# Kernel optimization log

Measured on AMD Instinct MI355X. Metric: run time of the kernel, lower is better.

The kernel has to match this reference:

```python
import jax, jax.numpy as jnp
import numpy as np

B, S, D = 8, 1024, 1024

def setup_inputs() -> dict:
    key = jax.random.key(0)
    ks = jax.random.split(key, 6)
    context = jax.random.normal(ks[0], (B, S, D), dtype=jnp.float32)
    eos_mask = jax.random.randint(ks[1], (B, S), 0, 2, dtype=jnp.int32)
    prior = jax.random.uniform(ks[2], (), dtype=jnp.float32)
    adj_mat = jax.random.randint(ks[3], (B, S, S), 0, 2, dtype=jnp.int32)
    Wk = jax.random.normal(ks[4], (D, D), dtype=jnp.float32) * 0.02
    Wq = jax.random.normal(ks[5], (D, D), dtype=jnp.float32) * 0.02
    bk = jnp.zeros((D,), jnp.float32)
    bq = jnp.zeros((D,), jnp.float32)
    ln_gamma = jnp.ones((D,), jnp.float32)
    ln_beta = jnp.zeros((D,), jnp.float32)
    return {"context": context, "eos_mask": eos_mask, "prior": prior,
            "adj_mat": adj_mat, "Wk": Wk, "bk": bk, "Wq": Wq, "bq": bq,
            "ln_gamma": ln_gamma, "ln_beta": ln_beta}

def reference(context, eos_mask, prior, adj_mat, Wk, bk, Wq, bq, ln_gamma, ln_beta):
    d_model = context.shape[-1]
    seq_len = context.shape[1]
    # LayerNorm (annotated-transformer style: unbiased std, eps added to std)
    mu = jnp.mean(context, axis=-1, keepdims=True)
    std = jnp.std(context, axis=-1, keepdims=True, ddof=1)
    x = ln_gamma * (context - mu) / (std + 1e-6) + ln_beta
    # projections (torch Linear: x @ W.T + b)
    key_p = x @ Wk.T + bk
    query = x @ Wq.T + bq
    scores = jnp.einsum('bqd,bkd->bqk', query, key_p) / (d_model / 2)
    scores = jnp.where(adj_mat == 0, -1e9, scores)
    neibor_attn = jax.nn.softmax(scores, axis=-1)
    neibor_attn = jnp.sqrt(neibor_attn * jnp.swapaxes(neibor_attn, -1, -2) + 1e-9)
    neibor_attn = prior + (1.0 - prior) * neibor_attn
    # constant structural matrices
    a = jnp.eye(seq_len, k=1, dtype=jnp.float32)          # superdiagonal
    b = jnp.eye(seq_len, dtype=jnp.float32)               # diagonal
    tri = jnp.triu(jnp.ones((seq_len, seq_len), jnp.float32))  # upper incl diag
    # t = (log(attn+eps) masked to superdiagonal) @ tri
    t = jnp.matmul(jnp.where(a == 0, 0.0, jnp.log(neibor_attn + 1e-9)), tri)
    g_attn = jnp.exp(jnp.matmul(tri, t))
    g_attn = jnp.where((tri - b) == 0, 0.0, g_attn)  # keep strict upper only
    g_attn = g_attn + jnp.swapaxes(g_attn, -1, -2) + jnp.where(b == 0, 1e-9, neibor_attn)
    return (g_attn, neibor_attn)
```

## Files before the change

### kernel.cpp

```cpp
#include <hip/hip_runtime.h>
#include <hip/hip_bf16.h>

#define S_LEN 1024
#define D_DIM 1024
#define N_BAT 8
#define BSS   (8ull*1024ull*1024ull)

using bf16x8 = __attribute__((ext_vector_type(8))) short;
using f32x4  = __attribute__((ext_vector_type(4))) float;

__device__ __forceinline__ short f2bf(float v) {
    __hip_bfloat16 h = __float2bfloat16(v);
    return *reinterpret_cast<short*>(&h);
}

__device__ __forceinline__ void gload_lds16(const void* g, void* l) {
    __builtin_amdgcn_global_load_lds(
        (const __attribute__((address_space(1))) void*)g,
        (__attribute__((address_space(3))) void*)l, 16, 0, 0);
}

template<int KITERS>
__device__ __forceinline__ void gemm_mainloop256(
    const short* __restrict__ A, const short* __restrict__ Bt,
    int brow, int bcol, int kstart,
    short* As, short* Bs, f32x4 acc[4][4])
{
    const int tid  = threadIdx.x;
    const int lane = tid & 63;
    const int w    = tid >> 6;
    const int wr   = w >> 1;
    const int wc   = w & 1;
    const int rsel = lane & 15;
    const int kb   = (lane >> 4) * 16;
    const int sw   = (rsel & 7) << 4;

    const int srow  = tid >> 3;
    const int scolb = ((tid & 7) * 16) ^ ((srow & 7) << 4);
    const int sdst  = tid * 16;

#pragma unroll
    for (int m = 0; m < 4; ++m)
#pragma unroll
        for (int n = 0; n < 4; ++n) acc[m][n] = 0.0f;

    auto stage = [&](int slot, int k0) {
        char* Ad = (char*)As + slot * 32768;
        char* Bd = (char*)Bs + slot * 16384;
#pragma unroll
        for (int c = 0; c < 4; ++c) {
            const int row = c * 64 + srow;
            gload_lds16((const char*)(A + (size_t)(brow + row) * 1024 + k0) + scolb,
                        Ad + c * 8192 + sdst);
        }
#pragma unroll
        for (int c = 0; c < 2; ++c) {
            const int row = c * 64 + srow;
            gload_lds16((const char*)(Bt + (size_t)(bcol + row) * 1024 + k0) + scolb,
                        Bd + c * 8192 + sdst);
        }
    };

    stage(0, kstart);
    if (KITERS > 1) stage(1, kstart + 64);

#pragma unroll
    for (int t = 0; t < KITERS; ++t) {
        if (t < KITERS - 1) asm volatile("s_waitcnt vmcnt(6)" ::: "memory");
        else                asm volatile("s_waitcnt vmcnt(0)" ::: "memory");
        __builtin_amdgcn_s_barrier();
        asm volatile("" ::: "memory");

        const char* Ac = (const char*)As + (t % 3) * 32768;
        const char* Bc = (const char*)Bs + (t % 3) * 16384;
        bf16x8 af[4][2], bfr[4][2];
#pragma unroll
        for (int m = 0; m < 4; ++m) {
            const int row = wr * 64 + m * 16 + rsel;
#pragma unroll
            for (int kk = 0; kk < 2; ++kk)
                af[m][kk] = *(const bf16x8*)&Ac[row * 128 + ((kk * 64 + kb) ^ sw)];
        }
#pragma unroll
        for (int n = 0; n < 4; ++n) {
            const int row = wc * 64 + n * 16 + rsel;
#pragma unroll
            for (int kk = 0; kk < 2; ++kk)
                bfr[n][kk] = *(const bf16x8*)&Bc[row * 128 + ((kk * 64 + kb) ^ sw)];
        }

        if (t + 2 < KITERS) stage((t + 2) % 3, kstart + (t + 2) * 64);

        __builtin_amdgcn_s_setprio(1);
#pragma unroll
        for (int kk = 0; kk < 2; ++kk)
#pragma unroll
            for (int m = 0; m < 4; ++m)
#pragma unroll
                for (int n = 0; n < 4; ++n)
                    acc[m][n] = __builtin_amdgcn_mfma_f32_16x16x32_bf16(
                        af[m][kk], bfr[n][kk], acc[m][n], 0, 0, 0);
        __builtin_amdgcn_s_setprio(0);
    }
}

__global__ __launch_bounds__(512) void gemm_bf16(
    const short* __restrict__ A, const short* __restrict__ Bt,
    short* __restrict__ C)
{
    __shared__ short As[3 * 16384];
    __shared__ short Bs[3 * 8192];
    const int flat = blockIdx.x + 32 * blockIdx.y;
    const int nid  = (flat & 7) * 32 + (flat >> 3);
    const int mx   = nid >> 3;
    const int ny   = nid & 7;
    const int brow = mx * 256, bcol = ny * 128;

    f32x4 acc[4][4];
    gemm_mainloop256<16>(A, Bt, brow, bcol, 0, As, Bs, acc);

    const int lane = threadIdx.x & 63;
    const int w    = threadIdx.x >> 6;
    const int wr   = w >> 1, wc = w & 1;
#pragma unroll
    for (int m = 0; m < 4; ++m)
#pragma unroll
        for (int n = 0; n < 4; ++n) {
            const int colg = bcol + wc * 64 + n * 16 + (lane & 15);
#pragma unroll
            for (int r = 0; r < 4; ++r) {
                const int rowg = brow + wr * 64 + m * 16 + ((lane >> 4) * 4 + r);
                C[(size_t)rowg * 1024 + colg] = f2bf(acc[m][n][r]);
            }
        }
}

__global__ __launch_bounds__(512) void gemm_scores(
    const short* __restrict__ Tm, const short* __restrict__ Xm,
    const float* __restrict__ p, const float* __restrict__ r2,
    const float* __restrict__ c0p, float* __restrict__ Sc)
{
    __shared__ short As[3 * 16384];
    __shared__ short Bs[3 * 8192];
    const int flat = blockIdx.x + 4 * blockIdx.y + 32 * blockIdx.z;
    const int nid  = (flat & 7) * 32 + (flat >> 3);
    const int b    = nid >> 5;
    const int rem  = nid & 31;
    const int mx   = rem & 3;
    const int ny   = rem >> 2;
    const short* A  = Tm + (size_t)b * 1024 * 1024;
    const short* Bt = Xm + (size_t)b * 1024 * 1024;
    const float* pb = p  + (size_t)b * 1024;
    const float* rb = r2 + (size_t)b * 1024;
    float* C = Sc + (size_t)b * 1024 * 1024;
    const int brow = mx * 256, bcol = ny * 128;

    f32x4 acc[4][4];
    gemm_mainloop256<16>(A, Bt, brow, bcol, 0, As, Bs, acc);

    const int lane = threadIdx.x & 63;
    const int w    = threadIdx.x >> 6;
    const int wr   = w >> 1, wc = w & 1;
    const float c0v = c0p[0];
#pragma unroll
    for (int m = 0; m < 4; ++m)
#pragma unroll
        for (int n = 0; n < 4; ++n) {
            const int colg = bcol + wc * 64 + n * 16 + (lane & 15);
            const float radd = rb[colg] + c0v;
#pragma unroll
            for (int r = 0; r < 4; ++r) {
                const int rowg = brow + wr * 64 + m * 16 + ((lane >> 4) * 4 + r);
                C[(size_t)rowg * 1024 + colg] =
                    (acc[m][n][r] + pb[rowg] + radd) * 0.001953125f;
            }
        }
}

__global__ __launch_bounds__(512) void gemm_splitk(
    const short* __restrict__ A, const short* __restrict__ Bt,
    float* __restrict__ P)
{
    __shared__ short As[3 * 16384];
    __shared__ short Bs[3 * 8192];
    const int brow = blockIdx.x * 256, bcol = blockIdx.y * 128;
    const int z = blockIdx.z;

    f32x4 acc[4][4];
    gemm_mainloop256<4>(A, Bt, brow, bcol, z * 256, As, Bs, acc);

    float* Pz = P + (size_t)z * 1024 * 1024;
    const int lane = threadIdx.x & 63;
    const int w    = threadIdx.x >> 6;
    const int wr   = w >> 1, wc = w & 1;
#pragma unroll
    for (int m = 0; m < 4; ++m)
#pragma unroll
        for (int n = 0; n < 4; ++n) {
            const int colg = bcol + wc * 64 + n * 16 + (lane & 15);
#pragma unroll
            for (int r = 0; r < 4; ++r) {
                const int rowg = brow + wr * 64 + m * 16 + ((lane >> 4) * 4 + r);
                Pz[(size_t)rowg * 1024 + colg] = acc[m][n][r];
            }
        }
}

__global__ __launch_bounds__(256) void reduce_m2t(
    const float* __restrict__ P, short* __restrict__ M)
{
    const int idx = blockIdx.x * 256 + threadIdx.x;
    const float4* P4 = (const float4*)P;
    float4 s = P4[idx];
    const float4 s1 = P4[idx + 262144];
    const float4 s2 = P4[idx + 524288];
    const float4 s3 = P4[idx + 786432];
    s.x += s1.x + s2.x + s3.x;
    s.y += s1.y + s2.y + s3.y;
    s.z += s1.z + s2.z + s3.z;
    s.w += s1.w + s2.w + s3.w;
    short4 o;
    o.x = f2bf(s.x); o.y = f2bf(s.y); o.z = f2bf(s.z); o.w = f2bf(s.w);
    ((short4*)M)[idx] = o;
}

__global__ __launch_bounds__(256) void bias_gemv1(
    const float* __restrict__ Wq, const float* __restrict__ Wk,
    const float* __restrict__ bk, const float* __restrict__ bq,
    float* __restrict__ pu, float* __restrict__ pv)
{
    __shared__ float su[8][128];
    __shared__ float sv[8][128];
    const int tx = threadIdx.x & 31;
    const int ty = threadIdx.x >> 5;
    const int colBase = blockIdx.x * 128;
    const int rowBase = blockIdx.y * 64;
    const int i = colBase + tx * 4;
    float4 au = {0,0,0,0}, av = {0,0,0,0};
#pragma unroll
    for (int jj = 0; jj < 8; ++jj) {
        const int j = rowBase + ty + jj * 8;
        const float bkv = bk[j], bqv = bq[j];
        const float4 wq = *(const float4*)&Wq[(size_t)j * 1024 + i];
        const float4 wk = *(const float4*)&Wk[(size_t)j * 1024 + i];
        au.x += wq.x * bkv; au.y += wq.y * bkv; au.z += wq.z * bkv; au.w += wq.w * bkv;
        av.x += wk.x * bqv; av.y += wk.y * bqv; av.z += wk.z * bqv; av.w += wk.w * bqv;
    }
    ((float4*)su[ty])[tx] = au;
    ((float4*)sv[ty])[tx] = av;
    __syncthreads();
    if (ty == 0) {
        float4 s1 = ((float4*)su[0])[tx];
        float4 s2 = ((float4*)sv[0])[tx];
#pragma unroll
        for (int k = 1; k < 8; ++k) {
            const float4 t1 = ((float4*)su[k])[tx];
            const float4 t2 = ((float4*)sv[k])[tx];
            s1.x += t1.x; s1.y += t1.y; s1.z += t1.z; s1.w += t1.w;
            s2.x += t2.x; s2.y += t2.y; s2.z += t2.z; s2.w += t2.w;
        }
        ((float4*)&pu[(size_t)blockIdx.y * 1024 + colBase])[tx] = s1;
        ((float4*)&pv[(size_t)blockIdx.y * 1024 + colBase])[tx] = s2;
    }
}

__global__ __launch_bounds__(256) void bias_gemv2(
    const float* __restrict__ pu, const float* __restrict__ pv,
    const float* __restrict__ bk, const float* __restrict__ bq,
    float* __restrict__ u, float* __restrict__ v, float* __restrict__ c0)
{
    __shared__ float sh[4];
    const int i = blockIdx.x * 256 + threadIdx.x;
    float su = 0.0f, sv = 0.0f;
#pragma unroll
    for (int k = 0; k < 16; ++k) {
        su += pu[k * 1024 + i];
        sv += pv[k * 1024 + i];
    }
    u[i] = su;
    v[i] = sv;
    if (blockIdx.x == 0) {
        const int t = threadIdx.x;
        const float4 a = ((const float4*)bq)[t];
        const float4 b = ((const float4*)bk)[t];
        float s = a.x*b.x + a.y*b.y + a.z*b.z + a.w*b.w;
        for (int off = 32; off > 0; off >>= 1) s += __shfl_down(s, off);
        const int lane = t & 63, w = t >> 6;
        if (lane == 0) sh[w] = s;
        __syncthreads();
        if (t == 0) c0[0] = sh[0] + sh[1] + sh[2] + sh[3];
    }
}

__global__ __launch_bounds__(256) void ln_kernel(
    const float* __restrict__ X, const float* __restrict__ gamma,
    const float* __restrict__ beta, const float* __restrict__ u,
    const float* __restrict__ v2, short* __restrict__ Y,
    float* __restrict__ p, float* __restrict__ r2)
{
    __shared__ float sh[16];
    const size_t row = blockIdx.x;
    const int t = threadIdx.x;
    float4 v = ((const float4*)(X + row * 1024))[t];
    float s  = v.x + v.y + v.z + v.w;
    float ss = v.x*v.x + v.y*v.y + v.z*v.z + v.w*v.w;
    for (int off = 32; off > 0; off >>= 1) {
        s  += __shfl_down(s, off);
        ss += __shfl_down(ss, off);
    }
    const int lane = t & 63, w = t >> 6;
    if (lane == 0) { sh[w] = s; sh[4 + w] = ss; }
    __syncthreads();
    if (t == 0) {
        float S  = sh[0] + sh[1] + sh[2] + sh[3];
        float SS = sh[4] + sh[5] + sh[6] + sh[7];
        float mu = S * (1.0f / 1024.0f);
        float var = fmaxf((SS - S * mu) * (1.0f / 1023.0f), 0.0f);
        sh[0] = mu;
        sh[1] = 1.0f / (sqrtf(var) + 1e-6f);
    }
    __syncthreads();
    const float mu = sh[0], inv = sh[1];
    float4 g  = ((const float4*)gamma)[t];
    float4 be = ((const float4*)beta)[t];
    float y0 = g.x * (v.x - mu) * inv + be.x;
    float y1 = g.y * (v.y - mu) * inv + be.y;
    float y2 = g.z * (v.z - mu) * inv + be.z;
    float y3 = g.w * (v.w - mu) * inv + be.w;
    short4 o;
    o.x = f2bf(y0); o.y = f2bf(y1); o.z = f2bf(y2); o.w = f2bf(y3);
    ((short4*)(Y + row * 1024))[t] = o;
    float4 uu = ((const float4*)u)[t];
    float4 vv = ((const float4*)v2)[t];
    float dp = y0*uu.x + y1*uu.y + y2*uu.z + y3*uu.w;
    float dr = y0*vv.x + y1*vv.y + y2*vv.z + y3*vv.w;
    for (int off = 32; off > 0; off >>= 1) {
        dp += __shfl_down(dp, off);
        dr += __shfl_down(dr, off);
    }
    if (lane == 0) { sh[8 + w] = dp; sh[12 + w] = dr; }
    __syncthreads();
    if (t == 0) {
        p[row]  = sh[8] + sh[9] + sh[10] + sh[11];
        r2[row] = sh[12] + sh[13] + sh[14] + sh[15];
    }
}

__global__ __launch_bounds__(256) void cvt_t_kernel(
    const float* __restrict__ Wq, const float* __restrict__ Wk,
    short* __restrict__ wqt, short* __restrict__ wkt)
{
    __shared__ float T[32][33];
    const float* src = blockIdx.z ? Wk : Wq;
    short* dst = blockIdx.z ? wkt : wqt;
    const int bi = blockIdx.x * 32, bj = blockIdx.y * 32;
    const int c = threadIdx.x & 31, r0 = threadIdx.x >> 5;
#pragma unroll
    for (int rr = 0; rr < 4; ++rr) {
        const int r = r0 + rr * 8;
        T[r][c] = src[(size_t)(bi + r) * 1024 + bj + c];
    }
    __syncthreads();
#pragma unroll
    for (int rr = 0; rr < 4; ++rr) {
        const int r = r0 + rr * 8;
        dst[(size_t)(bj + r) * 1024 + bi + c] = f2bf(T[c][r]);
    }
}

__global__ __launch_bounds__(256) void softmax_kernel(
    const float* __restrict__ Sc, const int* __restrict__ adj,
    float* __restrict__ At)
{
    __shared__ float sh[4];
    const size_t row = blockIdx.x;
    const int t = threadIdx.x;
    const float4 sv = ((const float4*)(Sc + row * 1024))[t];
    const int4   av = ((const int4*)(adj + row * 1024))[t];
    float m = -3.0e38f;
    if (av.x) m = fmaxf(m, sv.x);
    if (av.y) m = fmaxf(m, sv.y);
    if (av.z) m = fmaxf(m, sv.z);
    if (av.w) m = fmaxf(m, sv.w);
    for (int off = 32; off > 0; off >>= 1) m = fmaxf(m, __shfl_down(m, off));
    const int lane = t & 63, w = t >> 6;
    if (lane == 0) sh[w] = m;
    __syncthreads();
    const float M = fmaxf(fmaxf(sh[0], sh[1]), fmaxf(sh[2], sh[3]));
    __syncthreads();
    float e0 = av.x ? expf(sv.x - M) : 0.0f;
    float e1 = av.y ? expf(sv.y - M) : 0.0f;
    float e2 = av.z ? expf(sv.z - M) : 0.0f;
    float e3 = av.w ? expf(sv.w - M) : 0.0f;
    float s = e0 + e1 + e2 + e3;
    for (int off = 32; off > 0; off >>= 1) s += __shfl_down(s, off);
    if (lane == 0) sh[w] = s;
    __syncthreads();
    const float Sm = sh[0] + sh[1] + sh[2] + sh[3];
    float4 o;
    if (Sm > 0.0f) {
        const float inv = 1.0f / Sm;
        o.x = e0 * inv; o.y = e1 * inv; o.z = e2 * inv; o.w = e3 * inv;
    } else {
        o.x = o.y = o.z = o.w = 1.0f / 1024.0f;
    }
    ((float4*)(At + row * 1024))[t] = o;
}

__global__ __launch_bounds__(1024) void cum2_kernel(
    const float* __restrict__ At, const float* __restrict__ prior_p,
    double* __restrict__ cum)
{
    __shared__ double sh[1024];
    const int b = blockIdx.x;
    const int t = threadIdx.x;
    const float prior = *prior_p;
    const float om = 1.0f - prior;
    const float* attn = At + (size_t)b * 1024 * 1024;
    double v = 0.0;
    if (t >= 1) {
        const int k = t - 1;
        const float a1 = attn[(size_t)k * 1024 + (k + 1)];
        const float a2 = attn[(size_t)(k + 1) * 1024 + k];
        const float na = prior + om * sqrtf(a1 * a2 + 1e-9f);
        v = (double)logf(na + 1e-9f);
    }
    sh[t] = v;
    __syncthreads();
#pragma unroll
    for (int off = 1; off < 1024; off <<= 1) {
        const double add = (t >= off) ? sh[t - off] : 0.0;
        __syncthreads();
        sh[t] += add;
        __syncthreads();
    }
    cum[b * 1024 + t] = sh[t];
}

__global__ __launch_bounds__(256) void na_g_kernel(
    float* __restrict__ At, const float* __restrict__ prior_p,
    const double* __restrict__ cum, float* __restrict__ G)
{
    const int ti = blockIdx.x >> 5, tj = blockIdx.x & 31;
    if (tj < ti) return;
    const int b = blockIdx.y;
    const float prior = *prior_p;
    const float om = 1.0f - prior;
    float* base = At + (size_t)b * 1024 * 1024;
    float* gb   = G  + (size_t)b * 1024 * 1024;
    const double* cb = cum + (size_t)b * 1024;
    __shared__ float T1[32][33];
    __shared__ float T2[32][33];
    const int c = threadIdx.x & 31, r0 = threadIdx.x >> 5;
#pragma unroll
    for (int rr = 0; rr < 4; ++rr) {
        const int r = r0 + rr * 8;
        T1[r][c] = base[(size_t)(ti * 32 + r) * 1024 + tj * 32 + c];
        T2[r][c] = base[(size_t)(tj * 32 + r) * 1024 + ti * 32 + c];
    }
    __syncthreads();
#pragma unroll
    for (int rr = 0; rr < 4; ++rr) {
        const int r = r0 + rr * 8;
        const int R1 = ti * 32 + r, C1 = tj * 32 + c;
        const float na1 = prior + om * sqrtf(T1[r][c] * T2[c][r] + 1e-9f);
        base[(size_t)R1 * 1024 + C1] = na1;
        float g1;
        if (R1 == C1) g1 = na1;
        else {
            const int lo = min(R1, C1), hi = max(R1, C1);
            g1 = expf((float)(cb[hi] - cb[lo])) + 1e-9f;
        }
        gb[(size_t)R1 * 1024 + C1] = g1;
        const int R2 = tj * 32 + r, C2 = ti * 32 + c;
        const float na2 = prior + om * sqrtf(T2[r][c] * T1[c][r] + 1e-9f);
        base[(size_t)R2 * 1024 + C2] = na2;
        float g2;
        if (R2 == C2) g2 = na2;
        else {
            const int lo = min(R2, C2), hi = max(R2, C2);
            g2 = expf((float)(cb[hi] - cb[lo])) + 1e-9f;
        }
        gb[(size_t)R2 * 1024 + C2] = g2;
    }
}

extern "C" void kernel_launch(void* const* d_in, const int* in_sizes, int n_in,
                              void* d_out, int out_size, void* d_ws, size_t ws_size,
                              hipStream_t stream)
{
    const float* context = (const float*)d_in[0];
    const float* prior   = (const float*)d_in[2];
    const int*   adj     = (const int*)d_in[3];
    const float* Wk      = (const float*)d_in[4];
    const float* bk      = (const float*)d_in[5];
    const float* Wq      = (const float*)d_in[6];
    const float* bq      = (const float*)d_in[7];
    const float* gamma   = (const float*)d_in[8];
    const float* beta    = (const float*)d_in[9];

    float* out   = (float*)d_out;
    float* gout  = out;
    float* naout = out + BSS;

    char* ws = (char*)d_ws;
    short*  xb    = (short*)(ws);
    short*  wqt   = (short*)(ws + (16ull << 20));
    short*  wkt   = (short*)(ws + (18ull << 20));
    short*  m2t   = (short*)(ws + (20ull << 20));
    short*  tb    = (short*)(ws + (22ull << 20));
    float*  m2par = (float*)tb;
    double* cumd  = (double*)(ws + (38ull << 20));
    float*  uvec  = (float*)(ws + (38ull << 20) + (1ull << 16));
    float*  vvec  = uvec + 1024;
    float*  c0    = vvec + 1024;
    float*  pvec  = c0 + 64;
    float*  rvec  = pvec + 8192;
    float*  pu    = rvec + 8192;
    float*  pv    = pu + 16384;

    bias_gemv1<<<dim3(8, 16), 256, 0, stream>>>(Wq, Wk, bk, bq, pu, pv);
    bias_gemv2<<<4, 256, 0, stream>>>(pu, pv, bk, bq, uvec, vvec, c0);
    ln_kernel<<<8192, 256, 0, stream>>>(context, gamma, beta, uvec, vvec,
                                        xb, pvec, rvec);
    cvt_t_kernel<<<dim3(32, 32, 2), 256, 0, stream>>>(Wq, Wk, wqt, wkt);
    gemm_splitk<<<dim3(4, 8, 4), 512, 0, stream>>>(wkt, wqt, m2par);
    reduce_m2t<<<1024, 256, 0, stream>>>(m2par, m2t);
    gemm_bf16<<<dim3(32, 8), 512, 0, stream>>>(xb, m2t, tb);
    gemm_scores<<<dim3(4, 8, 8), 512, 0, stream>>>(tb, xb, pvec, rvec, c0, gout);
    softmax_kernel<<<8192, 256, 0, stream>>>(gout, adj, naout);
    cum2_kernel<<<8, 1024, 0, stream>>>(naout, prior, cumd);
    na_g_kernel<<<dim3(1024, 8), 256, 0, stream>>>(naout, prior, cumd, gout);
}
```

Measured before the change: 132.6 us.

## Fuse adjacency masking into scores GEMM and recompute softmax from row stats

The adjacency mask now goes into the scores GEMM epilogue, which writes -1e9 for masked entries. The softmax kernel is replaced by a row-statistics kernel that writes only the max and reciprocal sum per row. The cumulative-sum and final kernels rebuild the probabilities on the fly from the scores plus those stats. This removes one full write and re-read of the normalized attention matrix and the separate adjacency read in softmax, at the cost of extra expf work in the consumers. The NA/G kernel also remaps block indices to interleave batches, and fully masked rows now follow the reference's -1e9 semantics instead of the special-case path.

After: 123.2 us. 1.08x faster.

```diff
diff --git a/kernel.cpp b/kernel.cpp
--- a/kernel.cpp
+++ b/kernel.cpp
@@ -138,7 +138,8 @@
 __global__ __launch_bounds__(512) void gemm_scores(
     const short* __restrict__ Tm, const short* __restrict__ Xm,
     const float* __restrict__ p, const float* __restrict__ r2,
-    const float* __restrict__ c0p, float* __restrict__ Sc)
+    const float* __restrict__ c0p, const int* __restrict__ adj,
+    float* __restrict__ Sc)
 {
     __shared__ short As[3 * 16384];
     __shared__ short Bs[3 * 8192];
@@ -152,6 +153,7 @@
     const short* Bt = Xm + (size_t)b * 1024 * 1024;
     const float* pb = p  + (size_t)b * 1024;
     const float* rb = r2 + (size_t)b * 1024;
+    const int*   ab = adj + (size_t)b * 1024 * 1024;
     float* C = Sc + (size_t)b * 1024 * 1024;
     const int brow = mx * 256, bcol = ny * 128;
 
@@ -171,8 +173,9 @@
 #pragma unroll
             for (int r = 0; r < 4; ++r) {
                 const int rowg = brow + wr * 64 + m * 16 + ((lane >> 4) * 4 + r);
-                C[(size_t)rowg * 1024 + colg] =
-                    (acc[m][n][r] + pb[rowg] + radd) * 0.001953125f;
+                const size_t idx = (size_t)rowg * 1024 + colg;
+                const float val = (acc[m][n][r] + pb[rowg] + radd) * 0.001953125f;
+                C[idx] = ab[idx] ? val : -1e9f;
             }
         }
 }
@@ -368,60 +371,47 @@
     }
 }
 
-__global__ __launch_bounds__(256) void softmax_kernel(
-    const float* __restrict__ Sc, const int* __restrict__ adj,
-    float* __restrict__ At)
+__global__ __launch_bounds__(256) void rowstat_kernel(
+    const float* __restrict__ Sc, float2* __restrict__ stats)
 {
     __shared__ float sh[4];
     const size_t row = blockIdx.x;
     const int t = threadIdx.x;
     const float4 sv = ((const float4*)(Sc + row * 1024))[t];
-    const int4   av = ((const int4*)(adj + row * 1024))[t];
-    float m = -3.0e38f;
-    if (av.x) m = fmaxf(m, sv.x);
-    if (av.y) m = fmaxf(m, sv.y);
-    if (av.z) m = fmaxf(m, sv.z);
-    if (av.w) m = fmaxf(m, sv.w);
+    float m = fmaxf(fmaxf(sv.x, sv.y), fmaxf(sv.z, sv.w));
     for (int off = 32; off > 0; off >>= 1) m = fmaxf(m, __shfl_down(m, off));
     const int lane = t & 63, w = t >> 6;
     if (lane == 0) sh[w] = m;
     __syncthreads();
     const float M = fmaxf(fmaxf(sh[0], sh[1]), fmaxf(sh[2], sh[3]));
     __syncthreads();
-    float e0 = av.x ? expf(sv.x - M) : 0.0f;
-    float e1 = av.y ? expf(sv.y - M) : 0.0f;
-    float e2 = av.z ? expf(sv.z - M) : 0.0f;
-    float e3 = av.w ? expf(sv.w - M) : 0.0f;
-    float s = e0 + e1 + e2 + e3;
+    float s = expf(sv.x - M) + expf(sv.y - M) + expf(sv.z - M) + expf(sv.w - M);
     for (int off = 32; off > 0; off >>= 1) s += __shfl_down(s, off);
     if (lane == 0) sh[w] = s;
     __syncthreads();
-    const float Sm = sh[0] + sh[1] + sh[2] + sh[3];
-    float4 o;
-    if (Sm > 0.0f) {
-        const float inv = 1.0f / Sm;
-        o.x = e0 * inv; o.y = e1 * inv; o.z = e2 * inv; o.w = e3 * inv;
-    } else {
-        o.x = o.y = o.z = o.w = 1.0f / 1024.0f;
-    }
-    ((float4*)(At + row * 1024))[t] = o;
+    if (t == 0) {
+        const float Sm = sh[0] + sh[1] + sh[2] + sh[3];
+        stats[row] = make_float2(M, 1.0f / Sm);
+    }
 }
 
 __global__ __launch_bounds__(1024) void cum2_kernel(
-    const float* __restrict__ At, const float* __restrict__ prior_p,
-    double* __restrict__ cum)
+    const float* __restrict__ Sc, const float2* __restrict__ stats,
+    const float* __restrict__ prior_p, double* __restrict__ cum)
 {
     __shared__ double sh[1024];
     const int b = blockIdx.x;
     const int t = threadIdx.x;
     const float prior = *prior_p;
     const float om = 1.0f - prior;
-    const float* attn = At + (size_t)b * 1024 * 1024;
+    const float* sc = Sc + (size_t)b * 1024 * 1024;
+    const float2* st = stats + (size_t)b * 1024;
     double v = 0.0;
     if (t >= 1) {
         const int k = t - 1;
-        const float a1 = attn[(size_t)k * 1024 + (k + 1)];
-        const float a2 = attn[(size_t)(k + 1) * 1024 + k];
+        const float2 s1 = st[k], s2 = st[k + 1];
+        const float a1 = expf(sc[(size_t)k * 1024 + (k + 1)] - s1.x) * s1.y;
+        const float a2 = expf(sc[(size_t)(k + 1) * 1024 + k] - s2.x) * s2.y;
         const float na = prior + om * sqrtf(a1 * a2 + 1e-9f);
         v = (double)logf(na + 1e-9f);
     }
@@ -437,17 +427,22 @@
     cum[b * 1024 + t] = sh[t];
 }
 
-__global__ __launch_bounds__(256) void na_g_kernel(
-    float* __restrict__ At, const float* __restrict__ prior_p,
-    const double* __restrict__ cum, float* __restrict__ G)
-{
-    const int ti = blockIdx.x >> 5, tj = blockIdx.x & 31;
+__global__ __launch_bounds__(256) void na_g2_kernel(
+    float* __restrict__ Sc, const float2* __restrict__ stats,
+    const float* __restrict__ prior_p, const double* __restrict__ cum,
+    float* __restrict__ NA)
+{
+    const int flat = blockIdx.x + 1024 * blockIdx.y;
+    const int nid  = (flat & 7) * 1024 + (flat >> 3);
+    const int b    = nid >> 10;
+    const int tidx = nid & 1023;
+    const int ti = tidx >> 5, tj = tidx & 31;
     if (tj < ti) return;
-    const int b = blockIdx.y;
     const float prior = *prior_p;
     const float om = 1.0f - prior;
-    float* base = At + (size_t)b * 1024 * 1024;
-    float* gb   = G  + (size_t)b * 1024 * 1024;
+    float* sc = Sc + (size_t)b * 1024 * 1024;
+    float* na = NA + (size_t)b * 1024 * 1024;
+    const float2* st = stats + (size_t)b * 1024;
     const double* cb = cum + (size_t)b * 1024;
     __shared__ float T1[32][33];
     __shared__ float T2[32][33];
@@ -455,8 +450,10 @@
 #pragma unroll
     for (int rr = 0; rr < 4; ++rr) {
         const int r = r0 + rr * 8;
-        T1[r][c] = base[(size_t)(ti * 32 + r) * 1024 + tj * 32 + c];
-        T2[r][c] = base[(size_t)(tj * 32 + r) * 1024 + ti * 32 + c];
+        const int R1 = ti * 32 + r, R2 = tj * 32 + r;
+        const float2 s1 = st[R1], s2 = st[R2];
+        T1[r][c] = expf(sc[(size_t)R1 * 1024 + tj * 32 + c] - s1.x) * s1.y;
+        T2[r][c] = expf(sc[(size_t)R2 * 1024 + ti * 32 + c] - s2.x) * s2.y;
     }
     __syncthreads();
 #pragma unroll
@@ -464,24 +461,24 @@
         const int r = r0 + rr * 8;
         const int R1 = ti * 32 + r, C1 = tj * 32 + c;
         const float na1 = prior + om * sqrtf(T1[r][c] * T2[c][r] + 1e-9f);
-        base[(size_t)R1 * 1024 + C1] = na1;
+        na[(size_t)R1 * 1024 + C1] = na1;
         float g1;
         if (R1 == C1) g1 = na1;
         else {
             const int lo = min(R1, C1), hi = max(R1, C1);
             g1 = expf((float)(cb[hi] - cb[lo])) + 1e-9f;
         }
-        gb[(size_t)R1 * 1024 + C1] = g1;
+        sc[(size_t)R1 * 1024 + C1] = g1;
         const int R2 = tj * 32 + r, C2 = ti * 32 + c;
         const float na2 = prior + om * sqrtf(T2[r][c] * T1[c][r] + 1e-9f);
-        base[(size_t)R2 * 1024 + C2] = na2;
+        na[(size_t)R2 * 1024 + C2] = na2;
         float g2;
         if (R2 == C2) g2 = na2;
         else {
             const int lo = min(R2, C2), hi = max(R2, C2);
             g2 = expf((float)(cb[hi] - cb[lo])) + 1e-9f;
         }
-        gb[(size_t)R2 * 1024 + C2] = g2;
+        sc[(size_t)R2 * 1024 + C2] = g2;
     }
 }
 
@@ -518,6 +515,7 @@
     float*  rvec  = pvec + 8192;
     float*  pu    = rvec + 8192;
     float*  pv    = pu + 16384;
+    float2* statv = (float2*)(pv + 16384);
 
     bias_gemv1<<<dim3(8, 16), 256, 0, stream>>>(Wq, Wk, bk, bq, pu, pv);
     bias_gemv2<<<4, 256, 0, stream>>>(pu, pv, bk, bq, uvec, vvec, c0);
@@ -527,8 +525,10 @@
     gemm_splitk<<<dim3(4, 8, 4), 512, 0, stream>>>(wkt, wqt, m2par);
     reduce_m2t<<<1024, 256, 0, stream>>>(m2par, m2t);
     gemm_bf16<<<dim3(32, 8), 512, 0, stream>>>(xb, m2t, tb);
-    gemm_scores<<<dim3(4, 8, 8), 512, 0, stream>>>(tb, xb, pvec, rvec, c0, gout);
-    softmax_kernel<<<8192, 256, 0, stream>>>(gout, adj, naout);
-    cum2_kernel<<<8, 1024, 0, stream>>>(naout, prior, cumd);
-    na_g_kernel<<<dim3(1024, 8), 256, 0, stream>>>(naout, prior, cumd, gout);
-}
+    gemm_scores<<<dim3(4, 8, 8), 512, 0, stream>>>(tb, xb, pvec, rvec, c0,
+                                                   adj, gout);
+    rowstat_kernel<<<8192, 256, 0, stream>>>(gout, statv);
+    cum2_kernel<<<8, 1024, 0, stream>>>(gout, statv, prior, cumd);
+    na_g2_kernel<<<dim3(1024, 8), 256, 0, stream>>>(gout, statv, prior, cumd,
+                                                    naout);
+}
```
